# Kernel optimization log

Hardware: AMD Instinct MI355X
Metric: run time of the kernel (lower is better)

## Reference

```python
import jax, jax.numpy as jnp
import numpy as np
import math

N, L, S, H, E, D = 2, 2048, 2048, 16, 64, 64

def setup_inputs() -> dict:
    key = jax.random.key(0)
    kq, kk, kv = jax.random.split(key, 3)
    return {
        "queries": jax.random.normal(kq, (N, L, H, E), dtype=jnp.float32),
        "keys": jax.random.normal(kk, (N, S, H, E), dtype=jnp.float32),
        "values": jax.random.normal(kv, (N, S, H, D), dtype=jnp.float32),
        "attn_mask": jnp.zeros((L, S), dtype=jnp.float32),  # additive mask
    }

def reference(queries, keys, values, attn_mask):
    e = queries.shape[-1]
    softmax_temp = 1.0 / math.sqrt(e)  # self.softmax_temp is None -> 1/sqrt(E)
    # (N,L,H,E) x (N,S,H,E) -> (N,H,L,S)
    qk = jnp.einsum('nlhe,nshe->nhls', queries, keys)
    qk = qk + attn_mask  # additive mask broadcast over (N,H)
    att = jax.nn.softmax(softmax_temp * qk, axis=-1)
    # dropout rate 0.0 (eval) -> identity
    v = jnp.einsum('nhls,nshd->nlhd', att, values)
    return v
```

## Files before the change

kernel.cpp:

```cpp
#include <hip/hip_runtime.h>
#include <hip/hip_bf16.h>


typedef short bf16x8 __attribute__((ext_vector_type(8)));
typedef float f32x4 __attribute__((ext_vector_type(4)));

constexpr int Nb = 2, Lq = 2048, Sk = 2048, Hh = 16, Ee = 64, Dd = 64;
constexpr int BM = 128;
constexpr int BN = 64;
constexpr int NT = Sk / BN;
constexpr int PPITCH = 72;
constexpr float SCALE_LOG2E = 0.125f * 1.4426950408889634f;

__device__ __forceinline__ short f2bf(float f) {
  union { float f; unsigned u; } v; v.f = f;
  unsigned r = (v.u + 0x7fffu + ((v.u >> 16) & 1u)) >> 16;
  return (short)r;
}

__device__ __forceinline__ unsigned pack_bf16x2(float a, float b) {
  union { __hip_bfloat162 h; unsigned u; } v;
  float2 f; f.x = a; f.y = b;
  v.h = __float22bfloat162_rn(f);
  return v.u;
}

__device__ __forceinline__ void async_copy16(const void* g, void* l) {
  __builtin_amdgcn_global_load_lds(
      (const __attribute__((address_space(1))) unsigned int*)g,
      (__attribute__((address_space(3))) unsigned int*)l, 16, 0, 0);
}

__global__ __launch_bounds__(256) void prep_kv(const float* __restrict__ K,
                                               const float* __restrict__ V,
                                               short* __restrict__ dst) {
  int gid = blockIdx.x * 256 + threadIdx.x;
  int l = gid & 63;
  int chunkid = gid >> 6;
  int ch = chunkid & 15;
  int t  = (chunkid >> 4) & 31;
  int nh = chunkid >> 9;
  int n = nh >> 4, h = nh & 15;
  int c = l & 15, quad = l >> 4;

  bf16x8 o;
  if (ch < 8) {
    int sb = ch >> 1, kc = ch & 1;
    int s = t * 64 + sb * 16 + c;
    int e0 = kc * 32 + quad * 8;
    const float* p = K + (((size_t)n * Sk + s) * Hh + h) * Ee + e0;
    float4 x = *(const float4*)(p);
    float4 y = *(const float4*)(p + 4);
    o[0] = f2bf(x.x); o[1] = f2bf(x.y); o[2] = f2bf(x.z); o[3] = f2bf(x.w);
    o[4] = f2bf(y.x); o[5] = f2bf(y.y); o[6] = f2bf(y.z); o[7] = f2bf(y.w);
  } else {
    int db = (ch - 8) >> 1, kc = (ch - 8) & 1;
    int d = db * 16 + c;
    int s0 = t * 64 + kc * 32 + quad * 8;
    const float* p = V + (((size_t)n * Sk + s0) * Hh + h) * Dd + d;
#pragma unroll
    for (int j = 0; j < 8; ++j) o[j] = f2bf(p[(size_t)j * Hh * Dd]);
  }
  *(bf16x8*)(dst + (size_t)gid * 8) = o;
}

__global__ __launch_bounds__(256) void attn_fwd(
    const float* __restrict__ Q, const short* __restrict__ KVf,
    const float* __restrict__ Msk, float* __restrict__ Out)
{
  __shared__ short KV[2][16 * 512];
  __shared__ short Ps[4 * 32 * PPITCH];

  const int tid  = threadIdx.x;
  const int lane = tid & 63;
  const int w    = tid >> 6;
  const int quad = lane >> 4;
  const int c    = lane & 15;

  const int qt = blockIdx.x;
  const int nh = blockIdx.y;
  const int n  = nh >> 4;
  const int h  = nh & 15;

  const int row0 = qt * BM + w * 32;

  bf16x8 qfrag[2][2];
#pragma unroll
  for (int cb = 0; cb < 2; ++cb) {
    const float* qp = Q + (((size_t)n * Lq + (row0 + cb * 16 + c)) * Hh + h) * Ee;
#pragma unroll
    for (int kc = 0; kc < 2; ++kc) {
      const float* p = qp + kc * 32 + quad * 8;
      float4 x = *(const float4*)(p);
      float4 y = *(const float4*)(p + 4);
      bf16x8 f;
      f[0] = f2bf(x.x * SCALE_LOG2E); f[1] = f2bf(x.y * SCALE_LOG2E);
      f[2] = f2bf(x.z * SCALE_LOG2E); f[3] = f2bf(x.w * SCALE_LOG2E);
      f[4] = f2bf(y.x * SCALE_LOG2E); f[5] = f2bf(y.y * SCALE_LOG2E);
      f[6] = f2bf(y.z * SCALE_LOG2E); f[7] = f2bf(y.w * SCALE_LOG2E);
      qfrag[cb][kc] = f;
    }
  }

  f32x4 o[2][4];
#pragma unroll
  for (int cb = 0; cb < 2; ++cb)
#pragma unroll
    for (int db = 0; db < 4; ++db) { o[cb][db][0] = 0.f; o[cb][db][1] = 0.f; o[cb][db][2] = 0.f; o[cb][db][3] = 0.f; }
  float rs[2] = {0.f, 0.f};

  const short* kvt = KVf + (size_t)nh * NT * 16 * 512;
  const float* mq[2];
#pragma unroll
  for (int cb = 0; cb < 2; ++cb) mq[cb] = Msk + (size_t)(row0 + cb * 16 + c) * Sk;

  short* pw = &Ps[(w * 32) * PPITCH];

#pragma unroll
  for (int i = 0; i < 4; ++i) {
    int ch = w * 4 + i;
    async_copy16(kvt + ((size_t)ch * 512) + lane * 8, &KV[0][ch * 512 + lane * 8]);
  }
  __syncthreads();

  for (int t = 0; t < NT; ++t) {
    const int buf = t & 1;
    const int s0 = t * BN;

    if (t + 1 < NT) {
      const short* gt = kvt + (size_t)(t + 1) * 16 * 512;
#pragma unroll
      for (int i = 0; i < 4; ++i) {
        int ch = w * 4 + i;
        async_copy16(gt + ((size_t)ch * 512) + lane * 8, &KV[buf ^ 1][ch * 512 + lane * 8]);
      }
    }

    const short* kb = &KV[buf][0];

    f32x4 sacc[2][4];
#pragma unroll
    for (int cb = 0; cb < 2; ++cb)
#pragma unroll
      for (int sb = 0; sb < 4; ++sb) {
        float4 mv = *(const float4*)(mq[cb] + s0 + sb * 16 + quad * 4);
        sacc[cb][sb][0] = mv.x * SCALE_LOG2E; sacc[cb][sb][1] = mv.y * SCALE_LOG2E;
        sacc[cb][sb][2] = mv.z * SCALE_LOG2E; sacc[cb][sb][3] = mv.w * SCALE_LOG2E;
      }
#pragma unroll
    for (int kc = 0; kc < 2; ++kc) {
#pragma unroll
      for (int sb = 0; sb < 4; ++sb) {
        bf16x8 kfrag = *(const bf16x8*)&kb[(sb * 2 + kc) * 512 + lane * 8];
#pragma unroll
        for (int cb = 0; cb < 2; ++cb)
          sacc[cb][sb] = __builtin_amdgcn_mfma_f32_16x16x32_bf16(kfrag, qfrag[cb][kc], sacc[cb][sb], 0, 0, 0);
      }
    }

#pragma unroll
    for (int cb = 0; cb < 2; ++cb)
#pragma unroll
      for (int sb = 0; sb < 4; ++sb) {
        float p0 = __builtin_amdgcn_exp2f(sacc[cb][sb][0]);
        float p1 = __builtin_amdgcn_exp2f(sacc[cb][sb][1]);
        float p2 = __builtin_amdgcn_exp2f(sacc[cb][sb][2]);
        float p3 = __builtin_amdgcn_exp2f(sacc[cb][sb][3]);
        rs[cb] += (p0 + p1) + (p2 + p3);
        unsigned lo = pack_bf16x2(p0, p1);
        unsigned hi = pack_bf16x2(p2, p3);
        short* pr = &pw[(cb * 16 + c) * PPITCH + sb * 16 + quad * 4];
        *(unsigned*)(pr + 0) = lo;
        *(unsigned*)(pr + 2) = hi;
      }

#pragma unroll
    for (int kc = 0; kc < 2; ++kc) {
      bf16x8 pfrag[2];
#pragma unroll
      for (int cb = 0; cb < 2; ++cb)
        pfrag[cb] = *(const bf16x8*)&pw[(cb * 16 + c) * PPITCH + kc * 32 + quad * 8];
#pragma unroll
      for (int db = 0; db < 4; ++db) {
        bf16x8 vfrag = *(const bf16x8*)&kb[(8 + db * 2 + kc) * 512 + lane * 8];
#pragma unroll
        for (int cb = 0; cb < 2; ++cb)
          o[cb][db] = __builtin_amdgcn_mfma_f32_16x16x32_bf16(vfrag, pfrag[cb], o[cb][db], 0, 0, 0);
      }
    }

    __syncthreads();
  }

#pragma unroll
  for (int cb = 0; cb < 2; ++cb) {
    float v = rs[cb];
    v += __shfl_xor(v, 16, 64);
    v += __shfl_xor(v, 32, 64);
    float inv = 1.0f / v;
    float* op = Out + (((size_t)n * Lq + (row0 + cb * 16 + c)) * Hh + h) * Dd + quad * 4;
#pragma unroll
    for (int db = 0; db < 4; ++db) {
      float4 ov;
      ov.x = o[cb][db][0] * inv; ov.y = o[cb][db][1] * inv;
      ov.z = o[cb][db][2] * inv; ov.w = o[cb][db][3] * inv;
      *(float4*)(op + db * 16) = ov;
    }
  }
}

extern "C" void kernel_launch(void* const* d_in, const int* in_sizes, int n_in,
                              void* d_out, int out_size, void* d_ws, size_t ws_size,
                              hipStream_t stream) {
  const float* Q   = (const float*)d_in[0];
  const float* K   = (const float*)d_in[1];
  const float* V   = (const float*)d_in[2];
  const float* Msk = (const float*)d_in[3];
  float* Out = (float*)d_out;

  short* KVf = (short*)d_ws;

  prep_kv<<<dim3(Nb * Hh * NT * 16 * 64 / 256), dim3(256), 0, stream>>>(K, V, KVf);

  dim3 grid(Lq / BM, Nb * Hh);
  attn_fwd<<<grid, dim3(256), 0, stream>>>(Q, KVf, Msk, Out);
}
```

Baseline: 188.3 us.

## Precompute bf16 swizzled mask tiles and stream them via async LDS copies

The prep kernel now also converts the additive mask to pre-scaled bf16, tiled per query block and XOR-swizzled, and the attention kernel streams these tiles into double-buffered LDS alongside K/V instead of reading fp32 mask rows directly from global memory. The P staging buffer switches from a padded pitch to an XOR swizzle, and block IDs are remapped so consecutive blocks cover different heads that share the same mask tile, for better L2 reuse. This halves mask bytes and makes those loads asynchronous, at the cost of extra LDS use (lower occupancy), a bf16-rounded mask, and a larger prep pass.

```diff
diff --git a/kernel.cpp b/kernel.cpp
--- a/kernel.cpp
+++ b/kernel.cpp
@@ -3,13 +3,15 @@
 
 
 typedef short bf16x8 __attribute__((ext_vector_type(8)));
+typedef short short4v __attribute__((ext_vector_type(4)));
+typedef unsigned uint2v __attribute__((ext_vector_type(2)));
 typedef float f32x4 __attribute__((ext_vector_type(4)));
 
 constexpr int Nb = 2, Lq = 2048, Sk = 2048, Hh = 16, Ee = 64, Dd = 64;
 constexpr int BM = 128;
 constexpr int BN = 64;
 constexpr int NT = Sk / BN;
-constexpr int PPITCH = 72;
+constexpr int KVB = Nb * Hh * NT * 16 * 64 / 256;
 constexpr float SCALE_LOG2E = 0.125f * 1.4426950408889634f;
 
 __device__ __forceinline__ short f2bf(float f) {
@@ -31,45 +33,61 @@
       (__attribute__((address_space(3))) unsigned int*)l, 16, 0, 0);
 }
 
-__global__ __launch_bounds__(256) void prep_kv(const float* __restrict__ K,
-                                               const float* __restrict__ V,
-                                               short* __restrict__ dst) {
-  int gid = blockIdx.x * 256 + threadIdx.x;
-  int l = gid & 63;
-  int chunkid = gid >> 6;
-  int ch = chunkid & 15;
-  int t  = (chunkid >> 4) & 31;
-  int nh = chunkid >> 9;
-  int n = nh >> 4, h = nh & 15;
-  int c = l & 15, quad = l >> 4;
-
-  bf16x8 o;
-  if (ch < 8) {
-    int sb = ch >> 1, kc = ch & 1;
-    int s = t * 64 + sb * 16 + c;
-    int e0 = kc * 32 + quad * 8;
-    const float* p = K + (((size_t)n * Sk + s) * Hh + h) * Ee + e0;
-    float4 x = *(const float4*)(p);
-    float4 y = *(const float4*)(p + 4);
-    o[0] = f2bf(x.x); o[1] = f2bf(x.y); o[2] = f2bf(x.z); o[3] = f2bf(x.w);
-    o[4] = f2bf(y.x); o[5] = f2bf(y.y); o[6] = f2bf(y.z); o[7] = f2bf(y.w);
+__global__ __launch_bounds__(256) void prep_all(const float* __restrict__ K,
+                                                const float* __restrict__ V,
+                                                const float* __restrict__ M,
+                                                short* __restrict__ KVf,
+                                                short* __restrict__ Mg) {
+  if (blockIdx.x < KVB) {
+    int gid = blockIdx.x * 256 + threadIdx.x;
+    int l = gid & 63;
+    int chunkid = gid >> 6;
+    int ch = chunkid & 15;
+    int t  = (chunkid >> 4) & 31;
+    int nh = chunkid >> 9;
+    int n = nh >> 4, h = nh & 15;
+    int c = l & 15, quad = l >> 4;
+    bf16x8 o;
+    if (ch < 8) {
+      int sb = ch >> 1, kc = ch & 1;
+      int s = t * 64 + sb * 16 + c;
+      int e0 = kc * 32 + quad * 8;
+      const float* p = K + (((size_t)n * Sk + s) * Hh + h) * Ee + e0;
+      float4 x = *(const float4*)(p);
+      float4 y = *(const float4*)(p + 4);
+      o[0] = f2bf(x.x); o[1] = f2bf(x.y); o[2] = f2bf(x.z); o[3] = f2bf(x.w);
+      o[4] = f2bf(y.x); o[5] = f2bf(y.y); o[6] = f2bf(y.z); o[7] = f2bf(y.w);
+    } else {
+      int db = (ch - 8) >> 1, kc = (ch - 8) & 1;
+      int d = db * 16 + c;
+      int s0 = t * 64 + kc * 32 + quad * 8;
+      const float* p = V + (((size_t)n * Sk + s0) * Hh + h) * Dd + d;
+#pragma unroll
+      for (int j = 0; j < 8; ++j) o[j] = f2bf(p[(size_t)j * Hh * Dd]);
+    }
+    *(bf16x8*)(KVf + (size_t)gid * 8) = o;
   } else {
-    int db = (ch - 8) >> 1, kc = (ch - 8) & 1;
-    int d = db * 16 + c;
-    int s0 = t * 64 + kc * 32 + quad * 8;
-    const float* p = V + (((size_t)n * Sk + s0) * Hh + h) * Dd + d;
-#pragma unroll
-    for (int j = 0; j < 8; ++j) o[j] = f2bf(p[(size_t)j * Hh * Dd]);
-  }
-  *(bf16x8*)(dst + (size_t)gid * 8) = o;
+    int u = (blockIdx.x - KVB) * 256 + threadIdx.x;
+    int grow = u & 511;
+    int l = u >> 9;
+    int t = grow >> 4, g = grow & 15;
+    int qt = l >> 7, lloc = l & 127;
+    float4 mv = *(const float4*)(M + (size_t)l * Sk + grow * 4);
+    short4v o;
+    o[0] = f2bf(mv.x * SCALE_LOG2E); o[1] = f2bf(mv.y * SCALE_LOG2E);
+    o[2] = f2bf(mv.z * SCALE_LOG2E); o[3] = f2bf(mv.w * SCALE_LOG2E);
+    size_t dst = ((((size_t)qt * NT + t) * 128 + lloc) << 6) + ((g ^ (lloc & 15)) << 2);
+    *(short4v*)(Mg + dst) = o;
+  }
 }
 
 __global__ __launch_bounds__(256) void attn_fwd(
     const float* __restrict__ Q, const short* __restrict__ KVf,
-    const float* __restrict__ Msk, float* __restrict__ Out)
+    const short* __restrict__ Mg, float* __restrict__ Out)
 {
-  __shared__ short KV[2][16 * 512];
-  __shared__ short Ps[4 * 32 * PPITCH];
+  __shared__ short KV[2][8192];
+  __shared__ short Ms[2][8192];
+  __shared__ short Ps[4][2048];
 
   const int tid  = threadIdx.x;
   const int lane = tid & 63;
@@ -77,10 +95,12 @@
   const int quad = lane >> 4;
   const int c    = lane & 15;
 
-  const int qt = blockIdx.x;
-  const int nh = blockIdx.y;
-  const int n  = nh >> 4;
-  const int h  = nh & 15;
+  const int id   = blockIdx.x;
+  const int slot = id >> 3;
+  const int qt   = slot & 15;
+  const int nh   = (id & 7) * 4 + (slot >> 4);
+  const int n    = nh >> 4;
+  const int h    = nh & 15;
 
   const int row0 = qt * BM + w * 32;
 
@@ -109,30 +129,28 @@
     for (int db = 0; db < 4; ++db) { o[cb][db][0] = 0.f; o[cb][db][1] = 0.f; o[cb][db][2] = 0.f; o[cb][db][3] = 0.f; }
   float rs[2] = {0.f, 0.f};
 
-  const short* kvt = KVf + (size_t)nh * NT * 16 * 512;
-  const float* mq[2];
-#pragma unroll
-  for (int cb = 0; cb < 2; ++cb) mq[cb] = Msk + (size_t)(row0 + cb * 16 + c) * Sk;
-
-  short* pw = &Ps[(w * 32) * PPITCH];
+  const short* kvt = KVf + (size_t)nh * NT * 8192;
+  const short* mqt = Mg  + (size_t)qt * NT * 8192;
 
 #pragma unroll
   for (int i = 0; i < 4; ++i) {
     int ch = w * 4 + i;
-    async_copy16(kvt + ((size_t)ch * 512) + lane * 8, &KV[0][ch * 512 + lane * 8]);
+    async_copy16(kvt + ch * 512 + lane * 8, &KV[0][ch * 512 + lane * 8]);
+    async_copy16(mqt + ch * 512 + lane * 8, &Ms[0][ch * 512 + lane * 8]);
   }
   __syncthreads();
 
   for (int t = 0; t < NT; ++t) {
     const int buf = t & 1;
-    const int s0 = t * BN;
 
     if (t + 1 < NT) {
-      const short* gt = kvt + (size_t)(t + 1) * 16 * 512;
+      const short* gk = kvt + (size_t)(t + 1) * 8192;
+      const short* gm = mqt + (size_t)(t + 1) * 8192;
 #pragma unroll
       for (int i = 0; i < 4; ++i) {
         int ch = w * 4 + i;
-        async_copy16(gt + ((size_t)ch * 512) + lane * 8, &KV[buf ^ 1][ch * 512 + lane * 8]);
+        async_copy16(gk + ch * 512 + lane * 8, &KV[buf ^ 1][ch * 512 + lane * 8]);
+        async_copy16(gm + ch * 512 + lane * 8, &Ms[buf ^ 1][ch * 512 + lane * 8]);
       }
     }
 
@@ -143,10 +161,15 @@
     for (int cb = 0; cb < 2; ++cb)
 #pragma unroll
       for (int sb = 0; sb < 4; ++sb) {
-        float4 mv = *(const float4*)(mq[cb] + s0 + sb * 16 + quad * 4);
-        sacc[cb][sb][0] = mv.x * SCALE_LOG2E; sacc[cb][sb][1] = mv.y * SCALE_LOG2E;
-        sacc[cb][sb][2] = mv.z * SCALE_LOG2E; sacc[cb][sb][3] = mv.w * SCALE_LOG2E;
-      }
+        int row = w * 32 + cb * 16 + c;
+        int gp = ((4 * sb + quad) ^ c) * 4;
+        uint2v mv = *(const uint2v*)&Ms[buf][row * 64 + gp];
+        sacc[cb][sb][0] = __uint_as_float(mv.x << 16);
+        sacc[cb][sb][1] = __uint_as_float(mv.x & 0xffff0000u);
+        sacc[cb][sb][2] = __uint_as_float(mv.y << 16);
+        sacc[cb][sb][3] = __uint_as_float(mv.y & 0xffff0000u);
+      }
+
 #pragma unroll
     for (int kc = 0; kc < 2; ++kc) {
 #pragma unroll
@@ -167,19 +190,25 @@
         float p2 = __builtin_amdgcn_exp2f(sacc[cb][sb][2]);
         float p3 = __builtin_amdgcn_exp2f(sacc[cb][sb][3]);
         rs[cb] += (p0 + p1) + (p2 + p3);
-        unsigned lo = pack_bf16x2(p0, p1);
-        unsigned hi = pack_bf16x2(p2, p3);
-        short* pr = &pw[(cb * 16 + c) * PPITCH + sb * 16 + quad * 4];
-        *(unsigned*)(pr + 0) = lo;
-        *(unsigned*)(pr + 2) = hi;
+        uint2v pv;
+        pv.x = pack_bf16x2(p0, p1);
+        pv.y = pack_bf16x2(p2, p3);
+        int gp = ((4 * sb + quad) ^ c) * 4;
+        *(uint2v*)&Ps[w][(cb * 16 + c) * 64 + gp] = pv;
       }
 
 #pragma unroll
     for (int kc = 0; kc < 2; ++kc) {
       bf16x8 pfrag[2];
 #pragma unroll
-      for (int cb = 0; cb < 2; ++cb)
-        pfrag[cb] = *(const bf16x8*)&pw[(cb * 16 + c) * PPITCH + kc * 32 + quad * 8];
+      for (int cb = 0; cb < 2; ++cb) {
+        int G0 = 8 * kc + 2 * quad;
+        int ga = (G0 ^ c) * 4, gb = ((G0 + 1) ^ c) * 4;
+        union { uint2v u[2]; bf16x8 f; } uu;
+        uu.u[0] = *(const uint2v*)&Ps[w][(cb * 16 + c) * 64 + ga];
+        uu.u[1] = *(const uint2v*)&Ps[w][(cb * 16 + c) * 64 + gb];
+        pfrag[cb] = uu.f;
+      }
 #pragma unroll
       for (int db = 0; db < 4; ++db) {
         bf16x8 vfrag = *(const bf16x8*)&kb[(8 + db * 2 + kc) * 512 + lane * 8];
@@ -219,9 +248,9 @@
   float* Out = (float*)d_out;
 
   short* KVf = (short*)d_ws;
-
-  prep_kv<<<dim3(Nb * Hh * NT * 16 * 64 / 256), dim3(256), 0, stream>>>(K, V, KVf);
-
-  dim3 grid(Lq / BM, Nb * Hh);
-  attn_fwd<<<grid, dim3(256), 0, stream>>>(Q, KVf, Msk, Out);
-}
+  short* Mg  = KVf + (size_t)Nb * Hh * NT * 8192;
+
+  prep_all<<<dim3(KVB + 4096), dim3(256), 0, stream>>>(K, V, Msk, KVf, Mg);
+
+  attn_fwd<<<dim3((Lq / BM) * Nb * Hh), dim3(256), 0, stream>>>(Q, KVf, Mg, Out);
+}
```

Result: faster. 177.8 us (-5.6%).
